# Kernel optimization log

Hardware: AMD Instinct MI355X
Metric: run time of the kernel (lower is better)

## Reference

```python
import jax, jax.numpy as jnp
import numpy as np

B, A, SK, SQ, D = 1, 16, 2048, 2048, 128
IDM, L, R = 128, 1, 3
T_ANNEAL, t_ANNEAL = 10.0, 0.0


def setup_inputs() -> dict:
    key = jax.random.key(0)
    ks = jax.random.split(key, 7)
    return {
        "K": jax.random.normal(ks[0], (B, A, SK, D), dtype=jnp.float32),
        "Q": jax.random.normal(ks[1], (B, A, SQ, D), dtype=jnp.float32),
        "Wk": jax.random.normal(ks[2], (IDM, D), dtype=jnp.float32) * (1.0 / np.sqrt(D)),
        "bk": jax.random.normal(ks[3], (IDM,), dtype=jnp.float32) * 0.02,
        "Wq": jax.random.normal(ks[4], (IDM, D), dtype=jnp.float32) * (1.0 / np.sqrt(D)),
        "bq": jax.random.normal(ks[5], (IDM,), dtype=jnp.float32) * 0.02,
        "W": jax.random.normal(ks[6], (A, IDM, L * R), dtype=jnp.float32),
    }


def reference(K, Q, Wk, bk, Wq, bq, W):
    b, a, sk, d = K.shape
    sq = Q.shape[2]
    # uplift (aug_k=0 so aug_K is identity): Linear y = x @ W^T + b
    Klifted = jnp.einsum('basd,ed->base', K, Wk) + bk  # [b,a,sk,idm]
    Qlifted = jnp.einsum('basd,ed->base', Q, Wq) + bq  # [b,a,sq,idm]
    # soft quantize to hash codes via annealed tanh
    Kc = jnp.tanh(jnp.einsum('basd,ade->base', Klifted, W) / T_ANNEAL)  # [b,a,sk,L*R]
    Qc = jnp.tanh(jnp.einsum('basd,ade->base', Qlifted, W) / T_ANNEAL)  # [b,a,sq,L*R]
    Kc = Kc.reshape(b, a, sk, L, R)
    Qc = Qc.reshape(b, a, sq, L, R)
    # per-table agreement count, normalized by R -> [b,a,L,sq,sk]
    pc = jnp.einsum('baslr,batlr->balts', Kc, Qc) / R
    # annealed soft threshold
    pc = jax.nn.sigmoid((pc - t_ANNEAL) / T_ANNEAL) * pc
    # max over L hash tables -> [b,a,sq,sk]
    return jnp.max(pc, axis=2)
```

## Files before the change

### kernel.cpp

```cpp
#include <hip/hip_runtime.h>
#include <hip/hip_bf16.h>
#include <math.h>

#define A_    16
#define SK_   2048
#define SQ_   2048
#define D_    128
#define IDM_  128
#define R_    3
#define NROW_ (A_ * SK_)

#define WS_VK 0
#define WS_VQ 6144
#define WS_CK 12288
#define WS_CQ 12336
#define WS_KC 12384
#define WS_QC 110688

__global__ void fuse_weights_kernel(const float* __restrict__ Wk,
                                    const float* __restrict__ bk,
                                    const float* __restrict__ Wq,
                                    const float* __restrict__ bq,
                                    const float* __restrict__ W,
                                    float* __restrict__ ws) {
    int bid = blockIdx.x;
    int isQ = (bid >= A_ * R_) ? 1 : 0;
    int ar  = isQ ? bid - A_ * R_ : bid;
    int a = ar / R_;
    int r = ar % R_;
    const float* Wm = isQ ? Wq : Wk;
    const float* bm = isQ ? bq : bk;
    int d = threadIdx.x;
    float acc = 0.f, cacc = 0.f;
    for (int e = 0; e < IDM_; ++e) {
        float w = W[(a * IDM_ + e) * R_ + r];
        acc  += Wm[e * D_ + d] * w;
        cacc += bm[e] * w;
    }
    float* V = ws + (isQ ? WS_VQ : WS_VK);
    V[(a * R_ + r) * D_ + d] = acc;
    if (d == 0) ws[(isQ ? WS_CQ : WS_CK) + a * R_ + r] = cacc;
}

__global__ void codes_kernel(const float* __restrict__ K,
                             const float* __restrict__ Q,
                             float* __restrict__ ws) {
    __shared__ __align__(16) float sV[R_][D_];
    __shared__ float sc[R_];
    int blk = blockIdx.x;
    int isQ = (blk >= 128) ? 1 : 0;
    int rowBase = (isQ ? blk - 128 : blk) * 256;
    int a = rowBase >> 11;
    const float* V = ws + (isQ ? WS_VQ : WS_VK) + a * R_ * D_;
    const float* c = ws + (isQ ? WS_CQ : WS_CK) + a * R_;
    int tid = threadIdx.x;
    for (int i = tid; i < R_ * D_; i += 256) sV[i / D_][i % D_] = V[i];
    if (tid < R_) sc[tid] = c[tid];
    __syncthreads();

    int row = rowBase + tid;
    const float4* row4 = ((const float4*)(isQ ? Q : K)) + (size_t)row * (D_ / 4);
    float a0 = 0.f, a1 = 0.f, a2 = 0.f;
    const float4* v0p = (const float4*)sV[0];
    const float4* v1p = (const float4*)sV[1];
    const float4* v2p = (const float4*)sV[2];
#pragma unroll 8
    for (int d4 = 0; d4 < D_ / 4; ++d4) {
        float4 x  = row4[d4];
        float4 v0 = v0p[d4];
        float4 v1 = v1p[d4];
        float4 v2 = v2p[d4];
        a0 += x.x * v0.x + x.y * v0.y + x.z * v0.z + x.w * v0.w;
        a1 += x.x * v1.x + x.y * v1.y + x.z * v1.z + x.w * v1.w;
        a2 += x.x * v2.x + x.y * v2.y + x.z * v2.z + x.w * v2.w;
    }
    float* codes = ws + (isQ ? WS_QC : WS_KC);
    codes[0 * NROW_ + row] = tanhf((a0 + sc[0]) * 0.1f);
    codes[1 * NROW_ + row] = tanhf((a1 + sc[1]) * 0.1f);
    codes[2 * NROW_ + row] = tanhf((a2 + sc[2]) * 0.1f);
}

__global__ void pc_kernel(const float* __restrict__ ws, float* __restrict__ out) {
    const int TT = 64;
    int a  = blockIdx.z;
    int t0 = blockIdx.y * TT;
    int s0 = blockIdx.x * 1024;
    __shared__ float sQ[R_][TT];
    int tid = threadIdx.x;
    if (tid < R_ * TT) {
        int r = tid / TT, t = tid % TT;
        sQ[r][t] = ws[WS_QC + r * NROW_ + a * SQ_ + t0 + t];
    }
    __syncthreads();

    int s = s0 + tid * 4;
    const float* kc = ws + WS_KC + a * SK_;
    float4 k0 = *(const float4*)(kc + 0 * NROW_ + s);
    float4 k1 = *(const float4*)(kc + 1 * NROW_ + s);
    float4 k2 = *(const float4*)(kc + 2 * NROW_ + s);

    float4* ob = (float4*)out;
    size_t rowBase = ((size_t)(a * SQ_ + t0) * SK_ + s) >> 2;
    const float third = 1.0f / 3.0f;
#pragma unroll 4
    for (int t = 0; t < TT; ++t) {
        float q0 = sQ[0][t], q1 = sQ[1][t], q2 = sQ[2][t];
        float4 o;
        float p;
        p = (k0.x * q0 + k1.x * q1 + k2.x * q2) * third; o.x = p * (0.5f + 0.025f * p);
        p = (k0.y * q0 + k1.y * q1 + k2.y * q2) * third; o.y = p * (0.5f + 0.025f * p);
        p = (k0.z * q0 + k1.z * q1 + k2.z * q2) * third; o.z = p * (0.5f + 0.025f * p);
        p = (k0.w * q0 + k1.w * q1 + k2.w * q2) * third; o.w = p * (0.5f + 0.025f * p);
        ob[rowBase + (size_t)t * (SK_ / 4)] = o;
    }
}

extern "C" void kernel_launch(void* const* d_in, const int* in_sizes, int n_in,
                              void* d_out, int out_size, void* d_ws, size_t ws_size,
                              hipStream_t stream) {
    const float* K  = (const float*)d_in[0];
    const float* Q  = (const float*)d_in[1];
    const float* Wk = (const float*)d_in[2];
    const float* bk = (const float*)d_in[3];
    const float* Wq = (const float*)d_in[4];
    const float* bq = (const float*)d_in[5];
    const float* W  = (const float*)d_in[6];
    float* out = (float*)d_out;
    float* ws  = (float*)d_ws;

    fuse_weights_kernel<<<2 * A_ * R_, 128, 0, stream>>>(Wk, bk, Wq, bq, W, ws);
    codes_kernel<<<256, 256, 0, stream>>>(K, Q, ws);
    dim3 grid(SK_ / 1024, SQ_ / 64, A_);
    pc_kernel<<<grid, 256, 0, stream>>>(ws, out);
}
```

Before: 355.1 us.

## Use nontemporal output stores, halve pc tile, warp-cooperative codes projection

```diff
diff --git a/kernel.cpp b/kernel.cpp
--- a/kernel.cpp
+++ b/kernel.cpp
@@ -17,6 +17,8 @@
 #define WS_KC 12384
 #define WS_QC 110688
 
+typedef float nt4 __attribute__((ext_vector_type(4)));
+
 __global__ void fuse_weights_kernel(const float* __restrict__ Wk,
                                     const float* __restrict__ bk,
                                     const float* __restrict__ Wq,
@@ -32,6 +34,7 @@
     const float* bm = isQ ? bq : bk;
     int d = threadIdx.x;
     float acc = 0.f, cacc = 0.f;
+#pragma unroll 8
     for (int e = 0; e < IDM_; ++e) {
         float w = W[(a * IDM_ + e) * R_ + r];
         acc  += Wm[e * D_ + d] * w;
@@ -48,8 +51,8 @@
     __shared__ __align__(16) float sV[R_][D_];
     __shared__ float sc[R_];
     int blk = blockIdx.x;
-    int isQ = (blk >= 128) ? 1 : 0;
-    int rowBase = (isQ ? blk - 128 : blk) * 256;
+    int isQ = (blk >= 512) ? 1 : 0;
+    int rowBase = (isQ ? blk - 512 : blk) * 64;
     int a = rowBase >> 11;
     const float* V = ws + (isQ ? WS_VQ : WS_VK) + a * R_ * D_;
     const float* c = ws + (isQ ? WS_CQ : WS_CK) + a * R_;
@@ -58,38 +61,46 @@
     if (tid < R_) sc[tid] = c[tid];
     __syncthreads();
 
-    int row = rowBase + tid;
-    const float4* row4 = ((const float4*)(isQ ? Q : K)) + (size_t)row * (D_ / 4);
-    float a0 = 0.f, a1 = 0.f, a2 = 0.f;
-    const float4* v0p = (const float4*)sV[0];
-    const float4* v1p = (const float4*)sV[1];
-    const float4* v2p = (const float4*)sV[2];
-#pragma unroll 8
-    for (int d4 = 0; d4 < D_ / 4; ++d4) {
-        float4 x  = row4[d4];
-        float4 v0 = v0p[d4];
-        float4 v1 = v1p[d4];
-        float4 v2 = v2p[d4];
-        a0 += x.x * v0.x + x.y * v0.y + x.z * v0.z + x.w * v0.w;
-        a1 += x.x * v1.x + x.y * v1.y + x.z * v1.z + x.w * v1.w;
-        a2 += x.x * v2.x + x.y * v2.y + x.z * v2.z + x.w * v2.w;
+    int sub  = tid >> 5;
+    int lane = tid & 31;
+    const float* src = isQ ? Q : K;
+    float* codes = ws + (isQ ? WS_QC : WS_KC);
+    float4 v0 = ((const float4*)sV[0])[lane];
+    float4 v1 = ((const float4*)sV[1])[lane];
+    float4 v2 = ((const float4*)sV[2])[lane];
+    float bias = (lane < R_) ? sc[lane] : 0.f;
+
+#pragma unroll
+    for (int pass = 0; pass < 8; ++pass) {
+        int row = rowBase + pass * 8 + sub;
+        float4 x = ((const float4*)(src + (size_t)row * D_))[lane];
+        float a0 = x.x * v0.x + x.y * v0.y + x.z * v0.z + x.w * v0.w;
+        float a1 = x.x * v1.x + x.y * v1.y + x.z * v1.z + x.w * v1.w;
+        float a2 = x.x * v2.x + x.y * v2.y + x.z * v2.z + x.w * v2.w;
+#pragma unroll
+        for (int off = 16; off >= 1; off >>= 1) {
+            a0 += __shfl_xor(a0, off, 32);
+            a1 += __shfl_xor(a1, off, 32);
+            a2 += __shfl_xor(a2, off, 32);
+        }
+        if (lane < R_) {
+            float v = (lane == 0) ? a0 : (lane == 1) ? a1 : a2;
+            codes[lane * NROW_ + row] = tanhf((v + bias) * 0.1f);
+        }
     }
-    float* codes = ws + (isQ ? WS_QC : WS_KC);
-    codes[0 * NROW_ + row] = tanhf((a0 + sc[0]) * 0.1f);
-    codes[1 * NROW_ + row] = tanhf((a1 + sc[1]) * 0.1f);
-    codes[2 * NROW_ + row] = tanhf((a2 + sc[2]) * 0.1f);
 }
 
-__global__ void pc_kernel(const float* __restrict__ ws, float* __restrict__ out) {
-    const int TT = 64;
+__global__ __launch_bounds__(256)
+void pc_kernel(const float* __restrict__ ws, float* __restrict__ out) {
+    const int TT = 32;
     int a  = blockIdx.z;
     int t0 = blockIdx.y * TT;
     int s0 = blockIdx.x * 1024;
     __shared__ float sQ[R_][TT];
     int tid = threadIdx.x;
     if (tid < R_ * TT) {
-        int r = tid / TT, t = tid % TT;
-        sQ[r][t] = ws[WS_QC + r * NROW_ + a * SQ_ + t0 + t];
+        int r = tid >> 5, t = tid & 31;
+        sQ[r][t] = ws[WS_QC + r * NROW_ + a * SQ_ + t0 + t] * (1.0f / 3.0f);
     }
     __syncthreads();
 
@@ -99,19 +110,18 @@
     float4 k1 = *(const float4*)(kc + 1 * NROW_ + s);
     float4 k2 = *(const float4*)(kc + 2 * NROW_ + s);
 
-    float4* ob = (float4*)out;
-    size_t rowBase = ((size_t)(a * SQ_ + t0) * SK_ + s) >> 2;
-    const float third = 1.0f / 3.0f;
+    nt4* op = (nt4*)out + (((size_t)(a * SQ_ + t0) * SK_ + s) >> 2);
 #pragma unroll 4
     for (int t = 0; t < TT; ++t) {
         float q0 = sQ[0][t], q1 = sQ[1][t], q2 = sQ[2][t];
-        float4 o;
+        nt4 o;
         float p;
-        p = (k0.x * q0 + k1.x * q1 + k2.x * q2) * third; o.x = p * (0.5f + 0.025f * p);
-        p = (k0.y * q0 + k1.y * q1 + k2.y * q2) * third; o.y = p * (0.5f + 0.025f * p);
-        p = (k0.z * q0 + k1.z * q1 + k2.z * q2) * third; o.z = p * (0.5f + 0.025f * p);
-        p = (k0.w * q0 + k1.w * q1 + k2.w * q2) * third; o.w = p * (0.5f + 0.025f * p);
-        ob[rowBase + (size_t)t * (SK_ / 4)] = o;
+        p = k0.x * q0 + k1.x * q1 + k2.x * q2; o.x = p * (0.5f + 0.025f * p);
+        p = k0.y * q0 + k1.y * q1 + k2.y * q2; o.y = p * (0.5f + 0.025f * p);
+        p = k0.z * q0 + k1.z * q1 + k2.z * q2; o.z = p * (0.5f + 0.025f * p);
+        p = k0.w * q0 + k1.w * q1 + k2.w * q2; o.w = p * (0.5f + 0.025f * p);
+        __builtin_nontemporal_store(o, op);
+        op += SK_ / 4;
     }
 }
 
@@ -129,7 +139,7 @@
     float* ws  = (float*)d_ws;
 
     fuse_weights_kernel<<<2 * A_ * R_, 128, 0, stream>>>(Wk, bk, Wq, bq, W, ws);
-    codes_kernel<<<256, 256, 0, stream>>>(K, Q, ws);
-    dim3 grid(SK_ / 1024, SQ_ / 64, A_);
+    codes_kernel<<<1024, 256, 0, stream>>>(K, Q, ws);
+    dim3 grid(SK_ / 1024, SQ_ / 32, A_);
     pc_kernel<<<grid, 256, 0, stream>>>(ws, out);
 }
```

New measurement: 312.8 us. 1.14x faster.
